# Optimization experiments

Hardware: AMD Instinct MI355X
Metric: run time of the kernel (lower is better)

The kernel has to match this reference:

```python
import jax, jax.numpy as jnp
import numpy as np
import itertools

# ---- static config (mirrors args in init_kwargs) ----
BS = 4                        # num_processes
H, W = 480, 640               # frame_height, frame_width
NC = 16                       # num_sem_categories
C = 4 + NC                    # obs channels: RGB + depth + semantics
RES = 5                       # map_resolution (cm per cell)
ZRES = 5
MAP_CM = 4800 // 2            # map_size_cm // global_downscaling
M = MAP_CM // RES             # 480 local-map cells
VR = 100                      # vision_range
FOV = 79.0                    # hfov (deg)
DU = 1                        # du_scale
AGENT_H = 1.55 * 100.0        # camera_height * 100 (cm)
MAXH = int(360 / ZRES)        # 72
MINH = int(-40 / ZRES)        # -8
ZH = MAXH - MINH              # 80 height bins
MAP_THR, EXP_THR, CAT_THR = 1.0, 1.0, 5.0
DEG = 57.29577951308232
MIN_Z = int(5 / ZRES - MINH)                    # 9
MAX_Z = int((AGENT_H + 1 + 50) / ZRES - MINH)   # 49
XCAM = (W - 1.0) / 2.0
ZCAM = (H - 1.0) / 2.0
FOC = (W / 2.0) / np.tan(np.deg2rad(FOV / 2.0))


def _splat_feat_nd(feat, coords, grid_dims):
    # feat: (B,F,N) ; coords: (B,3,N) normalized to [-1,1] ; trilinear scatter-add
    B, Fc, N = feat.shape
    G = grid_dims[0] * grid_dims[1] * grid_dims[2]
    grid_flat = jnp.zeros((B, Fc, G), feat.dtype)
    pos_dim, wts_dim = [], []
    for d in range(3):
        gd = grid_dims[d]
        pos = coords[:, d, :] * (gd / 2.0) + gd / 2.0   # (B,N) voxel-space coord
        fl = jnp.floor(pos)
        pd, wd = [], []
        for ix in (0.0, 1.0):
            pos_ix = fl + ix
            safe = ((pos_ix > 0) & (pos_ix < gd)).astype(feat.dtype)
            wd.append((1.0 - jnp.abs(pos - pos_ix)) * safe)
            pd.append(pos_ix * safe)  # unsafe points dumped at index 0 with weight 0
        pos_dim.append(pd)
        wts_dim.append(wd)
    for ix_d in itertools.product((0, 1), (0, 1), (0, 1)):
        w = wts_dim[0][ix_d[0]] * wts_dim[1][ix_d[1]] * wts_dim[2][ix_d[2]]
        idx = jnp.zeros_like(w)
        for d in range(3):
            idx = idx * grid_dims[d] + pos_dim[d][ix_d[d]]
        idx = idx.astype(jnp.int32)                     # (B,N)
        vals = feat * w[:, None, :]                     # (B,F,N)
        grid_flat = jax.vmap(lambda g, i, v: g.at[:, i].add(v))(grid_flat, idx, vals)
    grid_flat = jnp.round(grid_flat)
    return grid_flat.reshape((B, Fc) + tuple(grid_dims))


def _affine_grid(theta, Hh, Ww):
    # align_corners=True base grid
    xs = jnp.linspace(-1.0, 1.0, Ww)
    ys = jnp.linspace(-1.0, 1.0, Hh)
    Xg, Yg = jnp.meshgrid(xs, ys)
    base = jnp.stack([Xg, Yg, jnp.ones_like(Xg)], -1)   # (H,W,3)
    return jnp.einsum('bij,hwj->bhwi', theta, base)     # (B,H,W,2)


def _grid_sample(img, grid):
    # bilinear, align_corners=True, zero padding; img (B,C,H,W), grid (B,Ho,Wo,2)
    B, Cc, Hh, Ww = img.shape
    x = (grid[..., 0] + 1.0) * 0.5 * (Ww - 1)
    y = (grid[..., 1] + 1.0) * 0.5 * (Hh - 1)
    x0 = jnp.floor(x)
    y0 = jnp.floor(y)
    wx1 = x - x0
    wy1 = y - y0

    def gather(ix, iy):
        valid = ((ix >= 0) & (ix <= Ww - 1) & (iy >= 0) & (iy <= Hh - 1)).astype(img.dtype)
        ixc = jnp.clip(ix, 0, Ww - 1).astype(jnp.int32)
        iyc = jnp.clip(iy, 0, Hh - 1).astype(jnp.int32)
        v = jax.vmap(lambda im, yy, xx: im[:, yy, xx])(img, iyc, ixc)  # (B,C,Ho,Wo)
        return v * valid[:, None]

    return (gather(x0, y0) * ((1 - wx1) * (1 - wy1))[:, None]
            + gather(x0 + 1, y0) * (wx1 * (1 - wy1))[:, None]
            + gather(x0, y0 + 1) * ((1 - wx1) * wy1)[:, None]
            + gather(x0 + 1, y0 + 1) * (wx1 * wy1)[:, None])


def _forward(obs, pose_obs, maps_last, poses_last, view_angles):
    bs = obs.shape[0]
    depth = obs[:, 3, ::DU, ::DU]                        # (B,h,w) depth in cm
    gx = jnp.arange(W, dtype=obs.dtype)[None, None, ::DU]
    gz = jnp.arange(H - 1, -1, -1, dtype=obs.dtype)[None, ::DU, None]
    Xp = (gx - XCAM) * depth / FOC
    Zp = (gz - ZCAM) * depth / FOC
    # rotate about x-axis by per-env view angle (deg), then lift by agent height
    a = jnp.deg2rad(view_angles)[:, None, None]
    ca, sa = jnp.cos(a), jnp.sin(a)
    Xv = Xp
    Yv = ca * depth - sa * Zp
    Zv = sa * depth + ca * Zp + AGENT_H
    # shift_loc rotation angle is pi/2 - pi/2 = 0 -> identity rot, only x shift
    Xv = Xv + VR * RES / 2.0
    # normalize to [-1,1] voxel coords
    xs = (Xv / RES - VR // 2.0) / VR * 2.0
    ys = (Yv / RES - VR // 2.0) / VR * 2.0
    zs = (Zv / ZRES - (MAXH + MINH) // 2.0) / (MAXH - MINH) * 2.0
    coords = jnp.stack([xs, ys, zs], 1).reshape(bs, 3, -1)   # (B,3,N)
    # features: channel 0 = ones (occupancy), rest = avg-pooled semantic masks
    sem = obs[:, 4:]
    pooled = sem.reshape(bs, NC, H // DU, DU, W // DU, DU).mean((3, 5))
    N = (H // DU) * (W // DU)
    feat = jnp.concatenate([jnp.ones((bs, 1, N), obs.dtype), pooled.reshape(bs, NC, N)], 1)
    voxels = _splat_feat_nd(feat, coords, (VR, VR, ZH)).swapaxes(2, 3)  # (B,1+NC,VR,VR,ZH)
    agg = voxels[..., MIN_Z:MAX_Z].sum(4)
    fp_map_pred = jnp.clip(agg[:, :1] / MAP_THR, 0.0, 1.0)
    fp_exp_pred = jnp.clip(voxels.sum(4)[:, :1] / EXP_THR, 0.0, 1.0)
    cat_pred = jnp.clip(agg[:, 1:] / CAT_THR, 0.0, 1.0)
    agent_view = jnp.zeros((bs, C, M, M), obs.dtype)
    x1 = M // 2 - VR // 2
    x2 = x1 + VR
    y1 = M // 2
    y2 = y1 + VR
    agent_view = agent_view.at[:, 0:1, y1:y2, x1:x2].set(fp_map_pred)
    agent_view = agent_view.at[:, 1:2, y1:y2, x1:x2].set(fp_exp_pred)
    agent_view = agent_view.at[:, 4:, y1:y2, x1:x2].set(cat_pred)
    # pose integration (get_new_pose_batch, note sequential in-place semantics)
    o = poses_last[:, 2] / DEG
    yy = poses_last[:, 1] + pose_obs[:, 0] * jnp.sin(o) + pose_obs[:, 1] * jnp.cos(o)
    xx = poses_last[:, 0] + pose_obs[:, 0] * jnp.cos(o) - pose_obs[:, 1] * jnp.sin(o)
    tt = poses_last[:, 2] + pose_obs[:, 2] * DEG
    tt = jnp.fmod(tt - 180.0, 360.0) + 180.0
    tt = jnp.fmod(tt + 180.0, 360.0) - 180.0
    current_poses = jnp.stack([xx, yy, tt], 1)
    # st_pose is detached in the original
    st = jax.lax.stop_gradient(current_poses)
    half = M // 2
    stx = -(st[:, 0] * 100.0 / RES - half) / half
    sty = -(st[:, 1] * 100.0 / RES - half) / half
    t = (90.0 - st[:, 2]) * np.pi / 180.0
    ct, s_t = jnp.cos(t), jnp.sin(t)
    zero, one = jnp.zeros_like(ct), jnp.ones_like(ct)
    theta1 = jnp.stack([jnp.stack([ct, -s_t, zero], 1), jnp.stack([s_t, ct, zero], 1)], 1)
    theta2 = jnp.stack([jnp.stack([one, zero, stx], 1), jnp.stack([zero, one, sty], 1)], 1)
    rotated = _grid_sample(agent_view, _affine_grid(theta1, M, M))
    translated = _grid_sample(rotated, _affine_grid(theta2, M, M))
    map_pred = jnp.maximum(maps_last, translated)
    # pose_pred aliases the in-place-updated poses_last in torch == current_poses
    return fp_map_pred, map_pred, current_poses, current_poses, translated


def setup_inputs() -> dict:
    key = jax.random.key(0)
    k1, k2, k3, k4 = jax.random.split(key, 4)
    obs = jax.random.uniform(k1, (BS, C, H, W), jnp.float32)
    obs = obs.at[:, 3].multiply(400.0)  # depth channel in cm, up to 4 m
    pose_obs = jax.random.uniform(k2, (BS, 3), jnp.float32) * 0.25
    maps_last = jax.random.uniform(k3, (BS, C, M, M), jnp.float32)
    poses_last = jax.random.uniform(k4, (BS, 3), jnp.float32)
    view_angles = jnp.zeros((BS,), jnp.float32)
    return {"obs": obs, "pose_obs": pose_obs, "maps_last": maps_last,
            "poses_last": poses_last, "view_angles": view_angles}


def reference(obs, pose_obs, maps_last, poses_last, view_angles):
    return _forward(obs, pose_obs, maps_last, poses_last, view_angles)
```

## Files before the change

kernel.cpp:

```cpp
#include <hip/hip_runtime.h>
#include <math.h>

#define BS 4
#define HH 480
#define WW 640
#define NPX (HH * WW)
#define NC 16
#define CHN 20
#define MM 480
#define VRD 100
#define ZHD 80
#define MINZ 9
#define MAXZ 49
#define CAP 8192

#define OFF0 0
#define OFF1 40000
#define OFF2 18472000
#define OFF3 18472012
#define OFF4 18472024
#define OFFM 28840000
#define OFFC 36113600
#define RECOFF 40000

__device__ __forceinline__ void pix2pos(int w, int h, float depth, float ca, float sa,
                                        float foc, float& px, float& py, float& pz) {
    float gx = (float)w;
    float gz = (float)(HH - 1 - h);
    float Xp = (gx - 319.5f) * depth / foc;
    float Zp = (gz - 239.5f) * depth / foc;
    float Yv = ca * depth - sa * Zp;
    float Zv = sa * depth + ca * Zp + 155.0f;
    float Xv = Xp + 250.0f;
    float xs = (Xv / 5.0f - 50.0f) / 100.0f * 2.0f;
    float ys = (Yv / 5.0f - 50.0f) / 100.0f * 2.0f;
    float zs = (Zv / 5.0f - 32.0f) / 80.0f * 2.0f;
    px = xs * 50.0f + 50.0f;
    py = ys * 50.0f + 50.0f;
    pz = zs * 40.0f + 40.0f;
}

__global__ __launch_bounds__(256) void bin_kernel(const float* __restrict__ obs,
                                                  const float* __restrict__ va,
                                                  int* __restrict__ cnt,
                                                  float2* __restrict__ rec,
                                                  float foc) {
    int idx = blockIdx.x * blockDim.x + threadIdx.x;
    if (idx >= BS * NPX) return;
    int b   = idx / NPX;
    int rem = idx % NPX;
    float depth = obs[((size_t)b * CHN + 3) * NPX + rem];
    int h = rem / WW, w = rem % WW;
    float a  = va[b] * 0.017453292519943295f;
    float ca = cosf(a), sa = sinf(a);
    float px, py, pz;
    pix2pos(w, h, depth, ca, sa, foc, px, py, pz);
    int f = (int)floorf(py);
    if (f < 0 || f > 99) return;
    int slot = atomicAdd(cnt + (b * VRD + f) * 16, 1);
    if (slot < CAP) {
        float2 r; r.x = __int_as_float(rem); r.y = depth;
        rec[(size_t)(b * VRD + f) * CAP + slot] = r;
    }
}

__global__ __launch_bounds__(256, 5) void slice_kernel(const float* __restrict__ obs,
                                                       const int* __restrict__ cnt,
                                                       const float2* __restrict__ rec,
                                                       const float* __restrict__ va,
                                                       float* __restrict__ maps,
                                                       float* __restrict__ out0,
                                                       float foc) {
    __shared__ float acc[8000];
    int bid  = blockIdx.x;
    int wgid = (bid & 7) * 450 + (bid >> 3);
    int b  = wgid / 900;
    int r_ = wgid % 900;
    int g  = r_ / 100;
    int s  = r_ % 100;
    int tid = threadIdx.x;
    for (int i = tid; i < 8000; i += 256) acc[i] = 0.0f;
    __syncthreads();

    bool isocc = (g == 8);
    float clo = isocc ? 1.0f : 9.0f;
    float chi = isocc ? 80.0f : 49.0f;
    int zbase = isocc ? 0 : 9;
    const float* sb = isocc ? (const float*)0 : obs + ((size_t)b * CHN + 4 + 2 * g) * NPX;

    float a  = va[b] * 0.017453292519943295f;
    float ca = cosf(a), sa = sinf(a);
    int sm1 = (s > 0) ? s - 1 : 0;
    int n0 = (s > 0) ? min(cnt[(b * VRD + sm1) * 16], CAP) : 0;
    int n1 = min(cnt[(b * VRD + s) * 16], CAP);
    const float2* g0 = rec + (size_t)(b * VRD + sm1) * CAP;
    const float2* g1 = rec + (size_t)(b * VRD + s) * CAP;
    int N = (s == 0) ? 0 : n0 + n1;
    float fs = (float)s;

    int nblk = (N + 1023) >> 10;
    for (int blk = 0; blk < nblk; blk++) {
        int base = (blk << 10) + tid;
        float2 rv[4]; bool vld[4];
        #pragma unroll
        for (int j = 0; j < 4; j++) {
            int t = base + (j << 8);
            vld[j] = (t < N);
            rv[j] = vld[j] ? ((t < n0) ? g0[t] : g1[t - n0]) : make_float2(0.0f, 0.0f);
        }
        int rm[4]; float px[4], py[4], pz[4]; bool act[4];
        #pragma unroll
        for (int j = 0; j < 4; j++) {
            rm[j] = __float_as_int(rv[j].x);
            pix2pos(rm[j] % WW, rm[j] / WW, rv[j].y, ca, sa, foc, px[j], py[j], pz[j]);
            float wy = 1.0f - fabsf(py[j] - fs);
            bool ok = vld[j] && (wy > 0.0f);
            ok = ok && (pz[j] > clo - 1.0f) && (pz[j] < chi);
            float fx = floorf(px[j]);
            ok = ok && (fx + 1.0f > 0.0f) && (fx < 100.0f);
            act[j] = ok;
        }
        float sv0[4], sv1[4];
        #pragma unroll
        for (int j = 0; j < 4; j++) {
            bool gth = !isocc && act[j];
            sv0[j] = gth ? sb[rm[j]] : 1.0f;
            sv1[j] = gth ? sb[rm[j] + NPX] : 1.0f;
        }
        #pragma unroll
        for (int j = 0; j < 4; j++) {
            if (!act[j]) continue;
            float wy = 1.0f - fabsf(py[j] - fs);
            float fx = floorf(px[j]), fz = floorf(pz[j]);
            #pragma unroll
            for (int i2 = 0; i2 < 2; i2++) {
                float cxp = fx + (float)i2;
                if (!(cxp > 0.0f && cxp < 100.0f)) continue;
                float wxy = wy * (1.0f - fabsf(px[j] - cxp));
                int xi = (int)cxp;
                #pragma unroll
                for (int k = 0; k < 2; k++) {
                    float czp = fz + (float)k;
                    if (czp < clo || czp >= chi) continue;
                    float w3 = wxy * (1.0f - fabsf(pz[j] - czp));
                    if (w3 == 0.0f) continue;
                    int zi = (int)czp - zbase;
                    if (isocc) {
                        atomicAdd(&acc[zi * VRD + xi], w3);
                    } else {
                        float* dst = &acc[(zi * VRD + xi) * 2];
                        atomicAdd(dst + 0, w3 * sv0[j]);
                        atomicAdd(dst + 1, w3 * sv1[j]);
                    }
                }
            }
        }
    }
    __syncthreads();

    if (!isocc) {
        for (int i = tid; i < VRD * 2; i += 256) {
            int x = i >> 1, c = i & 1;
            float ssum = 0.0f;
            #pragma unroll 8
            for (int z = 0; z < 40; z++) ssum += rintf(acc[(z * VRD + x) * 2 + c]);
            maps[((size_t)(b * 18 + 2 + 2 * g + c) * VRD + s) * VRD + x] =
                fminf(fmaxf(ssum * 0.2f, 0.0f), 1.0f);
        }
    } else {
        for (int x = tid; x < VRD; x += 256) {
            float s_all = 0.0f, s_agg = 0.0f;
            #pragma unroll 8
            for (int z = 0; z < ZHD; z++) {
                float r = rintf(acc[z * VRD + x]);
                s_all += r;
                if (z >= MINZ && z < MAXZ) s_agg += r;
            }
            float fm = fminf(fmaxf(s_agg, 0.0f), 1.0f);
            float fe = fminf(fmaxf(s_all, 0.0f), 1.0f);
            maps[((size_t)(b * 18 + 0) * VRD + s) * VRD + x] = fm;
            maps[((size_t)(b * 18 + 1) * VRD + s) * VRD + x] = fe;
            out0[((size_t)b * VRD + s) * VRD + x] = fm;
        }
    }
}

__device__ __forceinline__ void pose_params(const float* __restrict__ pose_obs,
                                            const float* __restrict__ poses_last,
                                            int b, float& ct, float& st,
                                            float& stx, float& sty) {
    const float DEG = 57.29577951308232f;
    float o  = poses_last[b*3+2] / DEG;
    float so = sinf(o), co = cosf(o);
    float yy = poses_last[b*3+1] + pose_obs[b*3+0]*so + pose_obs[b*3+1]*co;
    float xx = poses_last[b*3+0] + pose_obs[b*3+0]*co - pose_obs[b*3+1]*so;
    float tt = poses_last[b*3+2] + pose_obs[b*3+2]*DEG;
    tt = fmodf(tt - 180.0f, 360.0f) + 180.0f;
    tt = fmodf(tt + 180.0f, 360.0f) - 180.0f;
    stx = -((xx*100.0f/5.0f) - 240.0f) / 240.0f;
    sty = -((yy*100.0f/5.0f) - 240.0f) / 240.0f;
    float t = (90.0f - tt) * 0.017453292519943295f;
    ct = cosf(t); st = sinf(t);
}

__global__ __launch_bounds__(64) void pose_kernel(const float* __restrict__ pose_obs,
                                                  const float* __restrict__ poses_last,
                                                  float* __restrict__ out) {
    int b = threadIdx.x;
    if (b >= BS) return;
    const float DEG = 57.29577951308232f;
    float o  = poses_last[b*3+2] / DEG;
    float so = sinf(o), co = cosf(o);
    float yy = poses_last[b*3+1] + pose_obs[b*3+0]*so + pose_obs[b*3+1]*co;
    float xx = poses_last[b*3+0] + pose_obs[b*3+0]*co - pose_obs[b*3+1]*so;
    float tt = poses_last[b*3+2] + pose_obs[b*3+2]*DEG;
    tt = fmodf(tt - 180.0f, 360.0f) + 180.0f;
    tt = fmodf(tt + 180.0f, 360.0f) - 180.0f;
    out[OFF2 + b*3+0] = xx; out[OFF2 + b*3+1] = yy; out[OFF2 + b*3+2] = tt;
    out[OFF3 + b*3+0] = xx; out[OFF3 + b*3+1] = yy; out[OFF3 + b*3+2] = tt;
}

__global__ __launch_bounds__(256) void rotate_kernel(const float* __restrict__ maps,
                                                     const float* __restrict__ pose_obs,
                                                     const float* __restrict__ poses_last,
                                                     float* __restrict__ rot) {
    int idx = blockIdx.x * blockDim.x + threadIdx.x;
    if (idx >= BS * MM * MM) return;
    int b   = idx / (MM * MM);
    int rem = idx % (MM * MM);
    int y   = rem / MM;
    int x   = rem % MM;
    float ct, st, stx, sty;
    pose_params(pose_obs, poses_last, b, ct, st, stx, sty);
    float Xg = -1.0f + (float)x * (2.0f / 479.0f);
    float Yg = -1.0f + (float)y * (2.0f / 479.0f);
    float gx = ct * Xg - st * Yg;
    float gy = st * Xg + ct * Yg;
    float xf = (gx + 1.0f) * 0.5f * 479.0f;
    float yf = (gy + 1.0f) * 0.5f * 479.0f;
    float x0 = floorf(xf), y0 = floorf(yf);
    float fx = xf - x0, fy = yf - y0;
    float cw[4] = {(1.0f - fx) * (1.0f - fy), fx * (1.0f - fy),
                   (1.0f - fx) * fy,          fx * fy};
    float cx[4] = {x0, x0 + 1.0f, x0, x0 + 1.0f};
    float cy[4] = {y0, y0, y0 + 1.0f, y0 + 1.0f};
    float acc[18];
    #pragma unroll
    for (int m = 0; m < 18; m++) acc[m] = 0.0f;
    #pragma unroll
    for (int k = 0; k < 4; k++) {
        float fxk = cx[k], fyk = cy[k];
        if (!(fxk >= 0.0f && fxk <= 479.0f && fyk >= 0.0f && fyk <= 479.0f)) continue;
        int ix = (int)fxk, iy = (int)fyk;
        if (iy < 240 || iy >= 340 || ix < 190 || ix >= 290) continue;
        int mi = iy - 240, mj = ix - 190;
        float w = cw[k];
        const float* mp = maps + (size_t)b * 18 * VRD * VRD + mi * VRD + mj;
        #pragma unroll
        for (int m = 0; m < 18; m++) acc[m] += w * mp[(size_t)m * VRD * VRD];
    }
    size_t obase = ((size_t)b * CHN) * MM * MM + (size_t)y * MM + x;
    rot[obase + (size_t)0 * MM * MM] = acc[0];
    rot[obase + (size_t)1 * MM * MM] = acc[1];
    rot[obase + (size_t)2 * MM * MM] = 0.0f;
    rot[obase + (size_t)3 * MM * MM] = 0.0f;
    #pragma unroll
    for (int m = 2; m < 18; m++)
        rot[obase + (size_t)(m + 2) * MM * MM] = acc[m];
}

__global__ __launch_bounds__(256) void translate_kernel(const float* __restrict__ rot,
                                                        const float* __restrict__ pose_obs,
                                                        const float* __restrict__ poses_last,
                                                        float* __restrict__ tr) {
    int idx = blockIdx.x * blockDim.x + threadIdx.x;
    if (idx >= BS * MM * MM) return;
    int b   = idx / (MM * MM);
    int rem = idx % (MM * MM);
    int y   = rem / MM;
    int x   = rem % MM;
    float ct, st, stx, sty;
    pose_params(pose_obs, poses_last, b, ct, st, stx, sty);
    float Xg = -1.0f + (float)x * (2.0f / 479.0f);
    float Yg = -1.0f + (float)y * (2.0f / 479.0f);
    float xf = (Xg + stx + 1.0f) * 0.5f * 479.0f;
    float yf = (Yg + sty + 1.0f) * 0.5f * 479.0f;
    float x0 = floorf(xf), y0 = floorf(yf);
    float fx = xf - x0, fy = yf - y0;
    float cw[4] = {(1.0f - fx) * (1.0f - fy), fx * (1.0f - fy),
                   (1.0f - fx) * fy,          fx * fy};
    float cxs[4] = {x0, x0 + 1.0f, x0, x0 + 1.0f};
    float cys[4] = {y0, y0, y0 + 1.0f, y0 + 1.0f};
    bool vk[4]; int offk[4];
    #pragma unroll
    for (int k = 0; k < 4; k++) {
        vk[k] = (cxs[k] >= 0.0f && cxs[k] <= 479.0f && cys[k] >= 0.0f && cys[k] <= 479.0f);
        offk[k] = vk[k] ? ((int)cys[k] * MM + (int)cxs[k]) : 0;
    }
    #pragma unroll
    for (int c = 0; c < CHN; c++) {
        const float* rp = rot + ((size_t)b * CHN + c) * MM * MM;
        float v = 0.0f;
        #pragma unroll
        for (int k = 0; k < 4; k++)
            if (vk[k]) v += cw[k] * rp[offk[k]];
        tr[((size_t)b * CHN + c) * MM * MM + (size_t)y * MM + x] = v;
    }
}

__global__ __launch_bounds__(256) void max_kernel(const float* __restrict__ maps_last,
                                                  const float* __restrict__ tr,
                                                  float* __restrict__ mp) {
    int i = blockIdx.x * blockDim.x + threadIdx.x;
    int n4 = BS * CHN * MM * MM / 4;
    if (i >= n4) return;
    float4 a = ((const float4*)maps_last)[i];
    float4 t = ((const float4*)tr)[i];
    float4 r;
    r.x = fmaxf(a.x, t.x);
    r.y = fmaxf(a.y, t.y);
    r.z = fmaxf(a.z, t.z);
    r.w = fmaxf(a.w, t.w);
    ((float4*)mp)[i] = r;
}

extern "C" void kernel_launch(void* const* d_in, const int* in_sizes, int n_in,
                              void* d_out, int out_size, void* d_ws, size_t ws_size,
                              hipStream_t stream) {
    const float* obs         = (const float*)d_in[0];
    const float* pose_obs    = (const float*)d_in[1];
    const float* maps_last   = (const float*)d_in[2];
    const float* poses_last  = (const float*)d_in[3];
    const float* view_angles = (const float*)d_in[4];
    float* out = (float*)d_out;

    float*  maps  = out + OFFM;
    float2* rec   = (float2*)(out + RECOFF);
    int*    cnt   = (int*)(out + OFFC);

    hipMemsetAsync(cnt, 0, 6400 * sizeof(int), stream);

    const float foc = (float)(320.0 / tan(39.5 * M_PI / 180.0));

    int npix = BS * NPX;
    bin_kernel<<<(npix + 255) / 256, 256, 0, stream>>>(obs, view_angles, cnt, rec, foc);

    slice_kernel<<<dim3(VRD * BS * 9), 256, 0, stream>>>(obs, cnt, rec, view_angles,
                                                         maps, out + OFF0, foc);

    pose_kernel<<<1, 64, 0, stream>>>(pose_obs, poses_last, out);

    int nmap = BS * MM * MM;
    rotate_kernel<<<(nmap + 255) / 256, 256, 0, stream>>>(maps, pose_obs, poses_last,
                                                          out + OFF1);
    translate_kernel<<<(nmap + 255) / 256, 256, 0, stream>>>(out + OFF1, pose_obs,
                                                             poses_last, out + OFF4);
    int n4 = BS * CHN * MM * MM / 4;
    max_kernel<<<(n4 + 255) / 256, 256, 0, stream>>>(maps_last, out + OFF4, out + OFF1);
}
```

Before: 1.299 ms.

## Pre-gather semantics and geometry into binned SoA buffers, split points by height band

The binning kernel now computes voxel coordinates once, drops points outside the x range early, and splits points into two bins by height: an in-band set, for which px/py/pz and all 16 semantic channels are copied contiguously into per-slice SoA buffers, and an out-of-band set used only for the occupancy grid. The slice kernel then reads coalesced pre-gathered values instead of recomputing pix2pos and doing random gathers from obs, and semantic workgroups skip points outside the agent height band. The trade-off is much more write traffic in bin_kernel (16 channel copies per kept point) and a smaller per-bin capacity cap (4288), which could silently drop points in dense bins.

New measurement: 1.385 ms. 6.6% more time.

```diff
diff --git a/kernel.cpp b/kernel.cpp
--- a/kernel.cpp
+++ b/kernel.cpp
@@ -12,16 +12,19 @@
 #define ZHD 80
 #define MINZ 9
 #define MAXZ 49
-#define CAP 8192
+#define CAP 4288
+#define SLOTS (400 * CAP)
 
 #define OFF0 0
 #define OFF1 40000
 #define OFF2 18472000
 #define OFF3 18472012
 #define OFF4 18472024
-#define OFFM 28840000
-#define OFFC 36113600
-#define RECOFF 40000
+#define OFFSEM 40000
+#define OFFGEO (OFFSEM + 16 * SLOTS)
+#define OFFRB  (OFFGEO + 3 * SLOTS)
+#define OFFMAP (OFFRB + 2 * SLOTS)
+#define OFFCNT (OFFMAP + 720000)
 
 __device__ __forceinline__ void pix2pos(int w, int h, float depth, float ca, float sa,
                                         float foc, float& px, float& py, float& pz) {
@@ -42,8 +45,13 @@
 
 __global__ __launch_bounds__(256) void bin_kernel(const float* __restrict__ obs,
                                                   const float* __restrict__ va,
-                                                  int* __restrict__ cnt,
-                                                  float2* __restrict__ rec,
+                                                  int* __restrict__ cntA,
+                                                  int* __restrict__ cntB,
+                                                  float* __restrict__ gpx,
+                                                  float* __restrict__ gpy,
+                                                  float* __restrict__ gpz,
+                                                  float* __restrict__ sem,
+                                                  float2* __restrict__ recB,
                                                   float foc) {
     int idx = blockIdx.x * blockDim.x + threadIdx.x;
     if (idx >= BS * NPX) return;
@@ -55,18 +63,38 @@
     float ca = cosf(a), sa = sinf(a);
     float px, py, pz;
     pix2pos(w, h, depth, ca, sa, foc, px, py, pz);
-    int f = (int)floorf(py);
-    if (f < 0 || f > 99) return;
-    int slot = atomicAdd(cnt + (b * VRD + f) * 16, 1);
-    if (slot < CAP) {
-        float2 r; r.x = __int_as_float(rem); r.y = depth;
-        rec[(size_t)(b * VRD + f) * CAP + slot] = r;
-    }
-}
-
-__global__ __launch_bounds__(256, 5) void slice_kernel(const float* __restrict__ obs,
-                                                       const int* __restrict__ cnt,
-                                                       const float2* __restrict__ rec,
+    float ff = floorf(py);
+    if (!(ff >= 0.0f && ff < 100.0f)) return;
+    float fx = floorf(px);
+    if (!(fx + 1.0f > 0.0f && fx < 100.0f)) return;
+    int f = (int)ff;
+    bool aok = (pz >= 8.0f && pz < 49.0f);
+    bool bok = !aok && (pz >= 0.0f && pz < 80.0f);
+    if (aok) {
+        int slot = atomicAdd(cntA + (b * VRD + f) * 16, 1);
+        if (slot < CAP) {
+            int o = (b * VRD + f) * CAP + slot;
+            gpx[o] = px; gpy[o] = py; gpz[o] = pz;
+            const float* sp = obs + ((size_t)b * CHN + 4) * NPX + rem;
+            #pragma unroll
+            for (int c = 0; c < NC; c++) sem[(size_t)c * SLOTS + o] = sp[(size_t)c * NPX];
+        }
+    } else if (bok) {
+        int slot = atomicAdd(cntB + (b * VRD + f) * 16, 1);
+        if (slot < CAP) {
+            float2 r; r.x = __int_as_float(rem); r.y = depth;
+            recB[(b * VRD + f) * CAP + slot] = r;
+        }
+    }
+}
+
+__global__ __launch_bounds__(256, 5) void slice_kernel(const int* __restrict__ cntA,
+                                                       const int* __restrict__ cntB,
+                                                       const float* __restrict__ gpx,
+                                                       const float* __restrict__ gpy,
+                                                       const float* __restrict__ gpz,
+                                                       const float* __restrict__ sem,
+                                                       const float2* __restrict__ recB,
                                                        const float* __restrict__ va,
                                                        float* __restrict__ maps,
                                                        float* __restrict__ out0,
@@ -82,75 +110,133 @@
     for (int i = tid; i < 8000; i += 256) acc[i] = 0.0f;
     __syncthreads();
 
-    bool isocc = (g == 8);
-    float clo = isocc ? 1.0f : 9.0f;
-    float chi = isocc ? 80.0f : 49.0f;
-    int zbase = isocc ? 0 : 9;
-    const float* sb = isocc ? (const float*)0 : obs + ((size_t)b * CHN + 4 + 2 * g) * NPX;
-
-    float a  = va[b] * 0.017453292519943295f;
-    float ca = cosf(a), sa = sinf(a);
-    int sm1 = (s > 0) ? s - 1 : 0;
-    int n0 = (s > 0) ? min(cnt[(b * VRD + sm1) * 16], CAP) : 0;
-    int n1 = min(cnt[(b * VRD + s) * 16], CAP);
-    const float2* g0 = rec + (size_t)(b * VRD + sm1) * CAP;
-    const float2* g1 = rec + (size_t)(b * VRD + s) * CAP;
-    int N = (s == 0) ? 0 : n0 + n1;
-    float fs = (float)s;
-
-    int nblk = (N + 1023) >> 10;
-    for (int blk = 0; blk < nblk; blk++) {
-        int base = (blk << 10) + tid;
-        float2 rv[4]; bool vld[4];
-        #pragma unroll
-        for (int j = 0; j < 4; j++) {
-            int t = base + (j << 8);
-            vld[j] = (t < N);
-            rv[j] = vld[j] ? ((t < n0) ? g0[t] : g1[t - n0]) : make_float2(0.0f, 0.0f);
-        }
-        int rm[4]; float px[4], py[4], pz[4]; bool act[4];
-        #pragma unroll
-        for (int j = 0; j < 4; j++) {
-            rm[j] = __float_as_int(rv[j].x);
-            pix2pos(rm[j] % WW, rm[j] / WW, rv[j].y, ca, sa, foc, px[j], py[j], pz[j]);
-            float wy = 1.0f - fabsf(py[j] - fs);
-            bool ok = vld[j] && (wy > 0.0f);
-            ok = ok && (pz[j] > clo - 1.0f) && (pz[j] < chi);
-            float fx = floorf(px[j]);
-            ok = ok && (fx + 1.0f > 0.0f) && (fx < 100.0f);
-            act[j] = ok;
-        }
-        float sv0[4], sv1[4];
-        #pragma unroll
-        for (int j = 0; j < 4; j++) {
-            bool gth = !isocc && act[j];
-            sv0[j] = gth ? sb[rm[j]] : 1.0f;
-            sv1[j] = gth ? sb[rm[j] + NPX] : 1.0f;
-        }
-        #pragma unroll
-        for (int j = 0; j < 4; j++) {
-            if (!act[j]) continue;
-            float wy = 1.0f - fabsf(py[j] - fs);
-            float fx = floorf(px[j]), fz = floorf(pz[j]);
-            #pragma unroll
-            for (int i2 = 0; i2 < 2; i2++) {
-                float cxp = fx + (float)i2;
-                if (!(cxp > 0.0f && cxp < 100.0f)) continue;
-                float wxy = wy * (1.0f - fabsf(px[j] - cxp));
-                int xi = (int)cxp;
-                #pragma unroll
-                for (int k = 0; k < 2; k++) {
-                    float czp = fz + (float)k;
-                    if (czp < clo || czp >= chi) continue;
-                    float w3 = wxy * (1.0f - fabsf(pz[j] - czp));
-                    if (w3 == 0.0f) continue;
-                    int zi = (int)czp - zbase;
-                    if (isocc) {
-                        atomicAdd(&acc[zi * VRD + xi], w3);
-                    } else {
-                        float* dst = &acc[(zi * VRD + xi) * 2];
-                        atomicAdd(dst + 0, w3 * sv0[j]);
-                        atomicAdd(dst + 1, w3 * sv1[j]);
+    if (s > 0) {
+        float fs = (float)s;
+        int f0 = s - 1, f1 = s;
+        int a0 = min(cntA[(b * VRD + f0) * 16], CAP);
+        int a1 = min(cntA[(b * VRD + f1) * 16], CAP);
+        int base0 = (b * VRD + f0) * CAP;
+        int base1 = (b * VRD + f1) * CAP;
+        int NA = a0 + a1;
+
+        if (g < 8) {
+            const float* s0p = sem + (size_t)(2 * g) * SLOTS;
+            const float* s1p = sem + (size_t)(2 * g + 1) * SLOTS;
+            for (int base = tid; base < NA; base += 1024) {
+                int o[4]; bool vld[4];
+                #pragma unroll
+                for (int j = 0; j < 4; j++) {
+                    int t = base + (j << 8);
+                    vld[j] = (t < NA);
+                    int oo = (t < a0) ? (base0 + t) : (base1 + (t - a0));
+                    o[j] = vld[j] ? oo : base0;
+                }
+                float px[4], py[4], pz[4], v0[4], v1[4];
+                #pragma unroll
+                for (int j = 0; j < 4; j++) {
+                    px[j] = gpx[o[j]]; py[j] = gpy[o[j]]; pz[j] = gpz[o[j]];
+                    v0[j] = s0p[o[j]]; v1[j] = s1p[o[j]];
+                }
+                #pragma unroll
+                for (int j = 0; j < 4; j++) {
+                    if (!vld[j]) continue;
+                    float wy = 1.0f - fabsf(py[j] - fs);
+                    if (wy <= 0.0f) continue;
+                    float fx = floorf(px[j]), fz = floorf(pz[j]);
+                    #pragma unroll
+                    for (int i2 = 0; i2 < 2; i2++) {
+                        float cxp = fx + (float)i2;
+                        if (!(cxp > 0.0f && cxp < 100.0f)) continue;
+                        float wxy = wy * (1.0f - fabsf(px[j] - cxp));
+                        int xi = (int)cxp;
+                        #pragma unroll
+                        for (int k = 0; k < 2; k++) {
+                            float czp = fz + (float)k;
+                            if (czp < 9.0f || czp >= 49.0f) continue;
+                            float w3 = wxy * (1.0f - fabsf(pz[j] - czp));
+                            if (w3 == 0.0f) continue;
+                            float* dst = &acc[(((int)czp - MINZ) * VRD + xi) * 2];
+                            atomicAdd(dst + 0, w3 * v0[j]);
+                            atomicAdd(dst + 1, w3 * v1[j]);
+                        }
+                    }
+                }
+            }
+        } else {
+            for (int base = tid; base < NA; base += 1024) {
+                int o[4]; bool vld[4];
+                #pragma unroll
+                for (int j = 0; j < 4; j++) {
+                    int t = base + (j << 8);
+                    vld[j] = (t < NA);
+                    int oo = (t < a0) ? (base0 + t) : (base1 + (t - a0));
+                    o[j] = vld[j] ? oo : base0;
+                }
+                float px[4], py[4], pz[4];
+                #pragma unroll
+                for (int j = 0; j < 4; j++) {
+                    px[j] = gpx[o[j]]; py[j] = gpy[o[j]]; pz[j] = gpz[o[j]];
+                }
+                #pragma unroll
+                for (int j = 0; j < 4; j++) {
+                    if (!vld[j]) continue;
+                    float wy = 1.0f - fabsf(py[j] - fs);
+                    if (wy <= 0.0f) continue;
+                    float fx = floorf(px[j]), fz = floorf(pz[j]);
+                    #pragma unroll
+                    for (int i2 = 0; i2 < 2; i2++) {
+                        float cxp = fx + (float)i2;
+                        if (!(cxp > 0.0f && cxp < 100.0f)) continue;
+                        float wxy = wy * (1.0f - fabsf(px[j] - cxp));
+                        int xi = (int)cxp;
+                        #pragma unroll
+                        for (int k = 0; k < 2; k++) {
+                            float czp = fz + (float)k;
+                            if (czp < 1.0f || czp >= 80.0f) continue;
+                            float w3 = wxy * (1.0f - fabsf(pz[j] - czp));
+                            if (w3 == 0.0f) continue;
+                            atomicAdd(&acc[(int)czp * VRD + xi], w3);
+                        }
+                    }
+                }
+            }
+            float a_  = va[b] * 0.017453292519943295f;
+            float ca = cosf(a_), sa = sinf(a_);
+            int b0 = min(cntB[(b * VRD + f0) * 16], CAP);
+            int b1 = min(cntB[(b * VRD + f1) * 16], CAP);
+            int NB = b0 + b1;
+            for (int base = tid; base < NB; base += 1024) {
+                float2 rv[4]; bool vld[4];
+                #pragma unroll
+                for (int j = 0; j < 4; j++) {
+                    int t = base + (j << 8);
+                    vld[j] = (t < NB);
+                    int oo = (t < b0) ? (base0 + t) : (base1 + (t - b0));
+                    rv[j] = vld[j] ? recB[oo] : make_float2(0.0f, 0.0f);
+                }
+                #pragma unroll
+                for (int j = 0; j < 4; j++) {
+                    if (!vld[j]) continue;
+                    int rm = __float_as_int(rv[j].x);
+                    float px, py, pz;
+                    pix2pos(rm % WW, rm / WW, rv[j].y, ca, sa, foc, px, py, pz);
+                    float wy = 1.0f - fabsf(py - fs);
+                    if (wy <= 0.0f) continue;
+                    float fx = floorf(px), fz = floorf(pz);
+                    #pragma unroll
+                    for (int i2 = 0; i2 < 2; i2++) {
+                        float cxp = fx + (float)i2;
+                        if (!(cxp > 0.0f && cxp < 100.0f)) continue;
+                        float wxy = wy * (1.0f - fabsf(px - cxp));
+                        int xi = (int)cxp;
+                        #pragma unroll
+                        for (int k = 0; k < 2; k++) {
+                            float czp = fz + (float)k;
+                            if (czp < 1.0f || czp >= 80.0f) continue;
+                            float w3 = wxy * (1.0f - fabsf(pz - czp));
+                            if (w3 == 0.0f) continue;
+                            atomicAdd(&acc[(int)czp * VRD + xi], w3);
+                        }
                     }
                 }
             }
@@ -158,7 +244,7 @@
     }
     __syncthreads();
 
-    if (!isocc) {
+    if (g < 8) {
         for (int i = tid; i < VRD * 2; i += 256) {
             int x = i >> 1, c = i & 1;
             float ssum = 0.0f;
@@ -334,18 +420,25 @@
     const float* view_angles = (const float*)d_in[4];
     float* out = (float*)d_out;
 
-    float*  maps  = out + OFFM;
-    float2* rec   = (float2*)(out + RECOFF);
-    int*    cnt   = (int*)(out + OFFC);
-
-    hipMemsetAsync(cnt, 0, 6400 * sizeof(int), stream);
+    float*  sem   = out + OFFSEM;
+    float*  gpx   = out + OFFGEO;
+    float*  gpy   = out + OFFGEO + SLOTS;
+    float*  gpz   = out + OFFGEO + 2 * SLOTS;
+    float2* recB  = (float2*)(out + OFFRB);
+    float*  maps  = out + OFFMAP;
+    int*    cntA  = (int*)(out + OFFCNT);
+    int*    cntB  = cntA + 6400;
+
+    hipMemsetAsync(cntA, 0, 12800 * sizeof(int), stream);
 
     const float foc = (float)(320.0 / tan(39.5 * M_PI / 180.0));
 
     int npix = BS * NPX;
-    bin_kernel<<<(npix + 255) / 256, 256, 0, stream>>>(obs, view_angles, cnt, rec, foc);
-
-    slice_kernel<<<dim3(VRD * BS * 9), 256, 0, stream>>>(obs, cnt, rec, view_angles,
+    bin_kernel<<<(npix + 255) / 256, 256, 0, stream>>>(obs, view_angles, cntA, cntB,
+                                                       gpx, gpy, gpz, sem, recB, foc);
+
+    slice_kernel<<<dim3(VRD * BS * 9), 256, 0, stream>>>(cntA, cntB, gpx, gpy, gpz,
+                                                         sem, recB, view_angles,
                                                          maps, out + OFF0, foc);
 
     pose_kernel<<<1, 64, 0, stream>>>(pose_obs, poses_last, out);
```
